# Kernel tuning notes

Hardware: AMD Instinct MI355X
Metric: run time of the kernel (lower is better)

Reference implementation:

```python
import jax, jax.numpy as jnp
import numpy as np

BS = 8
SP_IN, DN_IN = 256, 128
SP_OUT, DN_OUT = 512, 256
N_STK, N_STK_PNT = 32, 64
COOR = 64
SP_NEAR, DN_NEAR = 2, 10
BN_EPS = 1e-5


def _act(x):
    return jax.nn.leaky_relu(x, 0.2)


def _bn(x, g, b, axes):
    # training-mode batch norm over `axes`, per channel (axis 1)
    m = x.mean(axes, keepdims=True)
    v = x.var(axes, keepdims=True)
    shp = [1] * x.ndim
    shp[1] = x.shape[1]
    return g.reshape(shp) * (x - m) * jax.lax.rsqrt(v + BN_EPS) + b.reshape(shp)


def _conv2d(x, w, b, stride, pad_w):
    # x [B,C,H,W], w [O,I,1,kw]
    y = jax.lax.conv_general_dilated(
        x, w, window_strides=stride, padding=[(0, 0), (pad_w, pad_w)],
        dimension_numbers=('NCHW', 'OIHW', 'NCHW'))
    return y + b[None, :, None, None]


def _sq_dist(a, b):
    # a [B,N,C], b [B,M,C] -> [B,N,M]
    return (jnp.sum(a * a, -1)[:, :, None] + jnp.sum(b * b, -1)[:, None, :]
            - 2.0 * jnp.einsum('bnc,bmc->bnm', a, b))


def _index_points(p, idx):
    # p [B,N,C], idx [B,...] -> [B,...,C]
    B = p.shape[0]
    bidx = jnp.arange(B).reshape((B,) + (1,) * (idx.ndim - 1))
    return p[bidx, idx]


def _fps(x, m):
    # deterministic farthest point sampling, start at index 0. x [B,N,D] -> [B,m]
    B, N, _ = x.shape
    bar = jnp.arange(B)

    def step(carry, _):
        dist, far = carry
        cen = x[bar, far]                       # [B,D]
        d = jnp.sum((x - cen[:, None, :]) ** 2, -1)
        dist = jnp.minimum(dist, d)
        return (dist, jnp.argmax(dist, -1).astype(jnp.int32)), far

    init = (jnp.full((B, N), 1e10, x.dtype), jnp.zeros((B,), jnp.int32))
    _, idx = jax.lax.scan(step, init, None, length=m)
    return idx.T  # [B,m]


def _gcn(x, W, b, g, be, k):
    # DGCNN-style EdgeConv: knn in feature space, edge feat [x_j - x_i, x_i],
    # shared 1x1 conv + BN + act, max over neighbors. x [B,C,N] -> [B,O,N]
    xt = jnp.transpose(x, (0, 2, 1))            # [B,N,C]
    d = _sq_dist(xt, xt)
    _, idx = jax.lax.top_k(-d, k)               # [B,N,k] (includes self)
    neigh = _index_points(xt, idx)              # [B,N,k,C]
    cen = xt[:, :, None, :]
    edge = jnp.concatenate([neigh - cen, jnp.broadcast_to(cen, neigh.shape)], -1)
    h = jnp.einsum('bnkc,oc->bonk', edge, W) + b[None, :, None, None]
    h = _act(_bn(h, g, be, (0, 2, 3)))
    return jnp.max(h, axis=3)                   # [B,O,N]


def _forward(sparse_fea, dense_fea, stk_coor,
             d2s_w, d2s_b, d2s_g, d2s_be,
             gsp_w, gsp_b, gsp_g, gsp_be,
             gdn_w, gdn_b, gdn_g, gdn_be,
             dcv_w, dcv_b, dcv_g, dcv_be):
    bs = sparse_fea.shape[0]
    dn4 = dense_fea.reshape(bs, DN_IN, N_STK, N_STK_PNT)

    # DenseToSparse: conv (1,3) valid, BN, act, max over points -> concat
    h = _act(_bn(_conv2d(dn4, d2s_w, d2s_b, (1, 1), 0), d2s_g, d2s_be, (0, 2, 3)))
    sp_from_dn = jnp.max(h, axis=3)                       # [bs,DN_IN,N_STK]
    union_sparse = jnp.concatenate([sparse_fea, sp_from_dn], 1)

    # SparseToDense: broadcast stroke feature onto its points -> concat
    dn_from_sp = jnp.repeat(sparse_fea[:, :, :, None], N_STK_PNT, axis=3)
    union_dense = jnp.concatenate([dn4, dn_from_sp], 1).reshape(
        bs, SP_IN + DN_IN, N_STK * N_STK_PNT)

    # graph updates
    union_sparse = _gcn(union_sparse, gsp_w, gsp_b, gsp_g, gsp_be, SP_NEAR)   # [bs,SP_OUT,N_STK]
    union_dense = _gcn(union_dense, gdn_w, gdn_b, gdn_g, gdn_be, DN_NEAR)     # [bs,DN_OUT,N_pnt]

    # DownSample: FPS over strokes, gather, strided conv halves point count
    fps_idx = _fps(stk_coor, N_STK // 2)                  # [bs,N_STK//2]
    stk_coor_s = _index_points(stk_coor, fps_idx)         # [bs,N_STK//2,COOR]
    sp = jnp.transpose(_index_points(jnp.transpose(union_sparse, (0, 2, 1)), fps_idx), (0, 2, 1))

    emb_d = union_dense.shape[1]
    dn = union_dense.reshape(bs, emb_d, N_STK, N_STK_PNT).transpose(0, 2, 3, 1)
    dn = dn.reshape(bs, N_STK, N_STK_PNT * emb_d)
    dn = _index_points(dn, fps_idx)                       # gather whole strokes
    dn = dn.reshape(bs, N_STK // 2, N_STK_PNT, emb_d).transpose(0, 3, 1, 2)
    dn = _act(_bn(_conv2d(dn, dcv_w, dcv_b, (1, 2), 1), dcv_g, dcv_be, (0, 2, 3)))
    dn = dn.reshape(bs, dn.shape[1], (N_STK // 2) * (N_STK_PNT // 2))
    return sp, dn, stk_coor_s


def setup_inputs() -> dict:
    key = jax.random.key(0)
    ks = jax.random.split(key, 8)
    C_u = SP_IN + DN_IN

    def rn(k, shape, s=0.05):
        return jax.random.normal(k, shape, jnp.float32) * s

    return {
        'sparse_fea': jax.random.normal(ks[0], (BS, SP_IN, N_STK), jnp.float32),
        'dense_fea': jax.random.normal(ks[1], (BS, DN_IN, N_STK * N_STK_PNT), jnp.float32),
        'stk_coor': jax.random.normal(ks[2], (BS, N_STK, COOR), jnp.float32),
        'd2s_w': rn(ks[3], (DN_IN, DN_IN, 1, 3)), 'd2s_b': jnp.zeros(DN_IN),
        'd2s_g': jnp.ones(DN_IN), 'd2s_be': jnp.zeros(DN_IN),
        'gsp_w': rn(ks[4], (SP_OUT, 2 * C_u)), 'gsp_b': jnp.zeros(SP_OUT),
        'gsp_g': jnp.ones(SP_OUT), 'gsp_be': jnp.zeros(SP_OUT),
        'gdn_w': rn(ks[5], (DN_OUT, 2 * C_u)), 'gdn_b': jnp.zeros(DN_OUT),
        'gdn_g': jnp.ones(DN_OUT), 'gdn_be': jnp.zeros(DN_OUT),
        'dcv_w': rn(ks[6], (DN_OUT, DN_OUT, 1, 3)), 'dcv_b': jnp.zeros(DN_OUT),
        'dcv_g': jnp.ones(DN_OUT), 'dcv_be': jnp.zeros(DN_OUT),
    }


def reference(sparse_fea, dense_fea, stk_coor,
              d2s_w, d2s_b, d2s_g, d2s_be,
              gsp_w, gsp_b, gsp_g, gsp_be,
              gdn_w, gdn_b, gdn_g, gdn_be,
              dcv_w, dcv_b, dcv_g, dcv_be):
    return _forward(sparse_fea, dense_fea, stk_coor,
                    d2s_w, d2s_b, d2s_g, d2s_be,
                    gsp_w, gsp_b, gsp_g, gsp_be,
                    gdn_w, gdn_b, gdn_g, gdn_be,
                    dcv_w, dcv_b, dcv_g, dcv_be)
```

## Files before the change

kernel.cpp:

```cpp
#include <hip/hip_runtime.h>

#define NPTS 2048
#define CUF 384

__device__ __forceinline__ float lrelu(float y){ return y>=0.f ? y : 0.2f*y; }

#define GLD16(g, l) __builtin_amdgcn_global_load_lds( \
    (const __attribute__((address_space(1))) void*)(g), \
    (__attribute__((address_space(3))) void*)(l), 16, 0, 0)

__global__ void k_build_xdn(const float* __restrict__ dense,
                            const float* __restrict__ sparse,
                            float* __restrict__ X){
  int b = blockIdx.y, ch = blockIdx.x;
  int t = threadIdx.x;
  __shared__ float tile[64*128];
  for (int k=0;k<32;k++){
    int f = t + k*256;
    int c = f>>6, j = f&63;
    tile[j*128 + c] = dense[((size_t)b*128 + c)*NPTS + ch*64 + j];
  }
  __syncthreads();
  for (int k=0;k<32;k++){
    int f = t + k*256;
    int j = f>>7, c = f&127;
    X[((size_t)b*NPTS + ch*64 + j)*CUF + c] = tile[f];
  }
  float v = sparse[((size_t)b*256 + t)*32 + ch];
  for (int j=0;j<64;j++) X[((size_t)b*NPTS + ch*64 + j)*CUF + 128 + t] = v;
}

__global__ void k_sn(const float* __restrict__ X, float* __restrict__ sn){
  int g = blockIdx.x*256 + threadIdx.x;
  if (g >= 8*NPTS) return;
  const float* row = X + (size_t)g*CUF;
  float blk[4];
  #pragma unroll
  for (int bI=0;bI<4;bI++){
    const float* p = row + bI*96;
    float r[8];
    #pragma unroll
    for (int l=0;l<8;l++) r[l] = __fmul_rn(p[l], p[l]);
    #pragma unroll 1
    for (int i=8;i<96;i+=8){
      #pragma unroll
      for (int l=0;l<8;l++) r[l] = __fadd_rn(r[l], __fmul_rn(p[i+l], p[i+l]));
    }
    float s01 = __fadd_rn(r[0], r[1]);
    float s23 = __fadd_rn(r[2], r[3]);
    float s45 = __fadd_rn(r[4], r[5]);
    float s67 = __fadd_rn(r[6], r[7]);
    blk[bI] = __fadd_rn(__fadd_rn(s01, s23), __fadd_rn(s45, s67));
  }
  sn[g] = __fadd_rn(__fadd_rn(blk[0], blk[1]), __fadd_rn(blk[2], blk[3]));
}

__global__ __launch_bounds__(256) void k_dist_tri(
    const float* __restrict__ X, float* __restrict__ Dot, int b_base){
  int z = blockIdx.z; int b = b_base + z;
  int t = threadIdx.x;
  int tx = t & 15, ty = t >> 4;
  int idx = blockIdx.x, rb = 0;
  while (idx >= 16 - rb){ idx -= 16 - rb; rb++; }
  int cb = rb + idx;
  __shared__ float U[8576];
  float* Xr = U;
  float* Xc = U + 4096;
  float* Ds = U;
  int r0 = rb*128;
  int c0 = cb*128;
  const size_t xb = (size_t)b*NPTS*CUF;
  const size_t zb = (size_t)z*NPTS*NPTS;

  int wv  = t >> 6;
  int sub = (t & 63) >> 3;
  int gs  = t & 7;
  int rowsA[4]; int swzA[4];
  #pragma unroll
  for (int cc=0;cc<4;cc++){
    int grp = wv*4 + cc;
    int row = grp*8 + sub;
    rowsA[cc] = row;
    swzA[cc] = 4*(gs ^ (row&7));
  }

  float acc[8][8];
  #pragma unroll
  for (int i=0;i<8;i++){
    #pragma unroll
    for (int j=0;j<8;j++) acc[i][j] = 0.f;
  }
  for (int kt=0; kt<12; kt++){
    int k0 = kt*32;
    __syncthreads();
    #pragma unroll
    for (int cc=0;cc<4;cc++){
      int grp = wv*4 + cc;
      GLD16(X + xb + (size_t)(r0+rowsA[cc])*CUF + k0 + swzA[cc], Xr + grp*256);
      GLD16(X + xb + (size_t)(c0+rowsA[cc])*CUF + k0 + swzA[cc], Xc + grp*256);
    }
    __syncthreads();
    #pragma unroll
    for (int kk=0; kk<32; kk+=4){
      int G = kk>>2;
      float4 aa[8], bb[8];
      #pragma unroll
      for (int i=0;i<8;i++){ int r = ty+16*i; aa[i] = *(const float4*)&Xr[r*32 + 4*(G ^ (r&7))]; }
      #pragma unroll
      for (int j=0;j<8;j++){ int r = tx+16*j; bb[j] = *(const float4*)&Xc[r*32 + 4*(G ^ (r&7))]; }
      #pragma unroll
      for (int i=0;i<8;i++){
        #pragma unroll
        for (int j=0;j<8;j++){
          float a_ = acc[i][j];
          a_ = fmaf(aa[i].x, bb[j].x, a_);
          a_ = fmaf(aa[i].y, bb[j].y, a_);
          a_ = fmaf(aa[i].z, bb[j].z, a_);
          a_ = fmaf(aa[i].w, bb[j].w, a_);
          acc[i][j] = a_;
        }
      }
    }
  }
  #pragma unroll
  for (int i=0;i<8;i++){
    size_t rbase = zb + (size_t)(r0 + ty + 16*i)*NPTS + c0;
    #pragma unroll
    for (int j=0;j<8;j++) Dot[rbase + tx + 16*j] = acc[i][j];
  }
  if (rb != cb){
    for (int h=0; h<2; h++){
      __syncthreads();
      #pragma unroll
      for (int i2=0;i2<4;i2++){
        #pragma unroll
        for (int j=0;j<8;j++){
          Ds[(tx+16*j)*67 + ty + 16*i2] = acc[h*4+i2][j];
        }
      }
      __syncthreads();
      for (int e=t; e<128*64; e+=256){
        int col = e>>6, rr = e&63;
        Dot[zb + (size_t)(c0+col)*NPTS + r0 + h*64 + rr] = Ds[col*67 + rr];
      }
    }
  }
}

__global__ __launch_bounds__(256) void k_sel(const float* __restrict__ Dot,
                                             const float* __restrict__ sn,
                                             int* __restrict__ idx, int b_base){
  int t = threadIdx.x;
  int lane = t & 63, w = t >> 6;
  int rglob = blockIdx.x*4 + w;
  int bb = rglob >> 11;
  int r  = rglob & 2047;
  int b  = b_base + bb;
  const float* drow = Dot + ((size_t)bb*NPTS + r)*NPTS;
  const float* snp  = sn + (size_t)b*NPTS;
  float snr = snp[r];
  unsigned long long key[32];
  #pragma unroll
  for (int k=0;k<8;k++){
    int cbase = k*256 + lane*4;
    float4 dd = *(const float4*)&drow[cbase];
    float4 ss = *(const float4*)&snp[cbase];
    float v0 = __fsub_rn(__fadd_rn(snr, ss.x), __fmul_rn(2.0f, dd.x));
    float v1 = __fsub_rn(__fadd_rn(snr, ss.y), __fmul_rn(2.0f, dd.y));
    float v2 = __fsub_rn(__fadd_rn(snr, ss.z), __fmul_rn(2.0f, dd.z));
    float v3 = __fsub_rn(__fadd_rn(snr, ss.w), __fmul_rn(2.0f, dd.w));
    float vv[4] = {v0, v1, v2, v3};
    #pragma unroll
    for (int u=0;u<4;u++){
      unsigned int bits = __float_as_uint(vv[u]);
      unsigned int flip = bits ^ ((unsigned int)((int)bits >> 31) | 0x80000000u);
      key[k*4+u] = ((unsigned long long)flip << 32) | (unsigned int)(cbase + u);
    }
  }
  unsigned long long last = 0ull;
  int out[10];
  #pragma unroll
  for (int q=0;q<10;q++){
    const unsigned long long INF = 0xFFFFFFFFFFFFFFFFull;
    unsigned long long m0[16];
    #pragma unroll
    for (int s=0;s<16;s++){
      unsigned long long a = (key[s]    > last) ? key[s]    : INF;
      unsigned long long c = (key[s+16] > last) ? key[s+16] : INF;
      m0[s] = (c < a) ? c : a;
    }
    #pragma unroll
    for (int s=0;s<8;s++) m0[s] = (m0[s+8] < m0[s]) ? m0[s+8] : m0[s];
    #pragma unroll
    for (int s=0;s<4;s++) m0[s] = (m0[s+4] < m0[s]) ? m0[s+4] : m0[s];
    m0[0] = (m0[2] < m0[0]) ? m0[2] : m0[0];
    m0[1] = (m0[3] < m0[1]) ? m0[3] : m0[1];
    unsigned long long m = (m0[1] < m0[0]) ? m0[1] : m0[0];
    #pragma unroll
    for (int sh=1; sh<64; sh<<=1){
      unsigned long long o = (unsigned long long)__shfl_xor((long long)m, sh, 64);
      m = (o < m) ? o : m;
    }
    last = m;
    out[q] = (int)(m & 0xFFFFFFFFull);
  }
  if (lane == 0){
    int* o = idx + ((size_t)b*NPTS + r)*10;
    #pragma unroll
    for (int q=0;q<10;q++) o[q] = out[q];
  }
}

__global__ void k_prepw2(const float* __restrict__ gdn_w, const float* __restrict__ gsp_w,
                         float* __restrict__ Wcd, float* __restrict__ Wcs){
  int g = blockIdx.x*256 + threadIdx.x;
  if (g < 512*CUF){
    int o = g / CUF, c = g % CUF;
    float v;
    if (o < 256) v = gdn_w[(size_t)o*768 + c];
    else { int oo = o - 256; v = gdn_w[(size_t)oo*768 + 384 + c] - gdn_w[(size_t)oo*768 + c]; }
    Wcd[g] = v;
  } else {
    int g2 = g - 512*CUF;
    if (g2 < 1024*CUF){
      int o = g2 / CUF, c = g2 % CUF;
      float v;
      if (o < 512) v = gsp_w[(size_t)o*768 + c];
      else { int oo = o - 512; v = gsp_w[(size_t)oo*768 + 384 + c] - gsp_w[(size_t)oo*768 + c]; }
      Wcs[g2] = v;
    }
  }
}

__global__ __launch_bounds__(256) void k_gemm_pq2(const float* __restrict__ A, const float* __restrict__ W,
                         const float* __restrict__ bias, float* __restrict__ OUT){
  int b = blockIdx.z, mb = blockIdx.y, ob = blockIdx.x;
  int t = threadIdx.x; int tx = t&15, ty = t>>4;
  __shared__ float Xa[4096];
  __shared__ float Xw[4096];
  int m0 = mb*128, o0 = ob*128;
  float acc[8][8];
  #pragma unroll
  for (int i=0;i<8;i++){
    #pragma unroll
    for (int j=0;j<8;j++) acc[i][j] = 0.f;
  }
  int wv  = t >> 6;
  int sub = (t & 63) >> 3;
  int gs  = t & 7;
  int rowsA[4]; int swzA[4];
  #pragma unroll
  for (int cc=0;cc<4;cc++){
    int grp = wv*4 + cc;
    int row = grp*8 + sub;
    rowsA[cc] = row;
    swzA[cc] = 4*(gs ^ (row&7));
  }
  for (int kt=0; kt<12; kt++){
    int k0 = kt*32;
    __syncthreads();
    #pragma unroll
    for (int cc=0;cc<4;cc++){
      int grp = wv*4 + cc;
      GLD16(A + ((size_t)b*NPTS + m0 + rowsA[cc])*CUF + k0 + swzA[cc], Xa + grp*256);
      GLD16(W + (size_t)(o0 + rowsA[cc])*CUF + k0 + swzA[cc], Xw + grp*256);
    }
    __syncthreads();
    #pragma unroll
    for (int kk=0; kk<32; kk+=4){
      int G = kk>>2;
      float4 aa[8], bb[8];
      #pragma unroll
      for (int i=0;i<8;i++){ int r = ty+16*i; aa[i] = *(const float4*)&Xa[r*32 + 4*(G ^ (r&7))]; }
      #pragma unroll
      for (int j=0;j<8;j++){ int r = tx+16*j; bb[j] = *(const float4*)&Xw[r*32 + 4*(G ^ (r&7))]; }
      #pragma unroll
      for (int i=0;i<8;i++){
        #pragma unroll
        for (int j=0;j<8;j++){
          float a_ = acc[i][j];
          a_ = fmaf(aa[i].x, bb[j].x, a_);
          a_ = fmaf(aa[i].y, bb[j].y, a_);
          a_ = fmaf(aa[i].z, bb[j].z, a_);
          a_ = fmaf(aa[i].w, bb[j].w, a_);
          acc[i][j] = a_;
        }
      }
    }
  }
  #pragma unroll
  for (int i=0;i<8;i++){
    int m = m0 + ty + 16*i;
    #pragma unroll
    for (int j=0;j<8;j++){
      int o = o0 + tx + 16*j;
      float v = acc[i][j];
      if (o >= 256) v += bias[o - 256];
      OUT[((size_t)b*NPTS + m)*512 + o] = v;
    }
  }
}

__global__ __launch_bounds__(256) void k_gemm_pq(const float* __restrict__ A, const float* __restrict__ W,
                         const float* __restrict__ bias,
                         float* __restrict__ OUT, int M, int Ototal, int Ohalf){
  int b = blockIdx.z, mb = blockIdx.y, ob = blockIdx.x;
  int t = threadIdx.x; int tr = t&15, tc = t>>4;
  __shared__ float At[64][68], Wt[64][68];
  int m0 = mb*64, o0 = ob*64;
  float acc[4][4];
  #pragma unroll
  for(int i=0;i<4;i++){
    #pragma unroll
    for(int j=0;j<4;j++) acc[i][j]=0.f;
  }
  int li = t>>2, lk = (t&3)*16;
  for (int kt=0;kt<6;kt++){
    int k0 = kt*64;
    {
      int m = m0 + li;
      if (m < M){
        const float4* p = (const float4*)(A + ((size_t)b*M + m)*CUF + k0 + lk);
        #pragma unroll
        for (int e=0;e<4;e++) *(float4*)&At[li][lk+e*4] = p[e];
      } else {
        float4 z = make_float4(0.f,0.f,0.f,0.f);
        #pragma unroll
        for (int e=0;e<4;e++) *(float4*)&At[li][lk+e*4] = z;
      }
      const float4* pw = (const float4*)(W + (size_t)(o0+li)*CUF + k0 + lk);
      #pragma unroll
      for (int e=0;e<4;e++) *(float4*)&Wt[li][lk+e*4] = pw[e];
    }
    __syncthreads();
    #pragma unroll
    for (int k4=0;k4<16;k4++){
      float4 aa[4], bb[4];
      aa[0] = *(const float4*)&At[tr   ][k4*4];
      aa[1] = *(const float4*)&At[tr+16][k4*4];
      aa[2] = *(const float4*)&At[tr+32][k4*4];
      aa[3] = *(const float4*)&At[tr+48][k4*4];
      bb[0] = *(const float4*)&Wt[tc   ][k4*4];
      bb[1] = *(const float4*)&Wt[tc+16][k4*4];
      bb[2] = *(const float4*)&Wt[tc+32][k4*4];
      bb[3] = *(const float4*)&Wt[tc+48][k4*4];
      #pragma unroll
      for(int i=0;i<4;i++){
        #pragma unroll
        for(int j=0;j<4;j++)
          acc[i][j] += aa[i].x*bb[j].x + aa[i].y*bb[j].y + aa[i].z*bb[j].z + aa[i].w*bb[j].w;
      }
    }
    __syncthreads();
  }
  #pragma unroll
  for(int i=0;i<4;i++){
    int m = m0 + tr + 16*i;
    if (m < M){
      #pragma unroll
      for(int j=0;j<4;j++){
        int o = o0 + tc + 16*j;
        float v = acc[i][j];
        if (o >= Ohalf) v += bias[o - Ohalf];
        OUT[((size_t)b*M + m)*Ototal + o] = v;
      }
    }
  }
}

__global__ __launch_bounds__(256) void k_gather_dn(const float* __restrict__ PQ, const int* __restrict__ idx,
                            float* __restrict__ dmax, float* __restrict__ dmin, double* __restrict__ part){
  int b = blockIdx.y, nb = blockIdx.x; int t = threadIdx.x;
  __shared__ int sidx[640];
  int n0 = nb*64;
  for (int k=t; k<640; k+=256) sidx[k] = idx[((size_t)b*NPTS + n0)*10 + k] & 2047;
  __syncthreads();
  double s=0.0, s2=0.0;
  const size_t pb = (size_t)b*NPTS*512;
  for (int n=0;n<64;n++){
    float qv = PQ[pb + (size_t)(n0+n)*512 + 256 + t];
    float mx = -3.4e38f, mn = 3.4e38f;
    #pragma unroll
    for (int k=0;k<10;k++){
      int m = sidx[n*10+k];
      float h = PQ[pb + (size_t)m*512 + t] + qv;
      mx = fmaxf(mx,h); mn = fminf(mn,h);
      s += h; s2 += (double)h*(double)h;
    }
    dmax[((size_t)b*NPTS + n0+n)*256 + t] = mx;
    dmin[((size_t)b*NPTS + n0+n)*256 + t] = mn;
  }
  size_t blk = (size_t)b*32 + nb;
  part[(blk*256 + t)*2] = s; part[(blk*256 + t)*2+1] = s2;
}

__global__ void k_reduce(const double* __restrict__ part, float* __restrict__ mv,
                         int nblk, int C, int count){
  int c = blockIdx.x; int t = threadIdx.x;
  double s=0.0, s2=0.0;
  for (int k=t;k<nblk;k+=64){ s += part[((size_t)k*C+c)*2]; s2 += part[((size_t)k*C+c)*2+1]; }
  #pragma unroll
  for (int off=32; off>=1; off>>=1){ s += __shfl_down(s, off, 64); s2 += __shfl_down(s2, off, 64); }
  if (t==0){
    double mean = s / (double)count;
    double var = s2 / (double)count - mean*mean;
    mv[c*2] = (float)mean;
    mv[c*2+1] = (float)(1.0 / sqrt(var + 1e-5));
  }
}

__global__ void k_epi(const float* __restrict__ xmin, float* __restrict__ xmax,
                      const float* __restrict__ mv, const float* __restrict__ g,
                      const float* __restrict__ be, int C, size_t total){
  size_t i = (size_t)blockIdx.x*256 + threadIdx.x;
  if (i>=total) return;
  int c = (int)(i % (size_t)C);
  float gg = g[c];
  float x = gg >= 0.f ? xmax[i] : xmin[i];
  float y = gg*(x - mv[c*2])*mv[c*2+1] + be[c];
  xmax[i] = lrelu(y);
}

__global__ __launch_bounds__(128) void k_d2s(const float* __restrict__ dense,
                      const float* __restrict__ w, const float* __restrict__ bias,
                      float* __restrict__ mx, float* __restrict__ mn, double* __restrict__ part){
  int b = blockIdx.y, s = blockIdx.x; int t = threadIdx.x;
  __shared__ float IN[128*64];
  for (int k=0;k<64;k++){
    int f = t + k*128;
    int ci = f>>6, wj = f&63;
    IN[f] = dense[((size_t)b*128 + ci)*NPTS + s*64 + wj];
  }
  __syncthreads();
  float acc[62];
  float bv = bias[t];
  #pragma unroll
  for (int wj=0;wj<62;wj++) acc[wj]=bv;
  for (int ci=0;ci<128;ci++){
    const float* wp = w + ((size_t)t*128 + ci)*3;
    float w0 = wp[0], w1 = wp[1], w2 = wp[2];
    const float* row = &IN[ci*64];
    #pragma unroll
    for (int wj=0;wj<62;wj++) acc[wj] += row[wj]*w0 + row[wj+1]*w1 + row[wj+2]*w2;
  }
  float vmx=-3.4e38f, vmn=3.4e38f; double ss=0.0, ss2=0.0;
  #pragma unroll
  for (int wj=0;wj<62;wj++){ float v = acc[wj]; vmx=fmaxf(vmx,v); vmn=fminf(vmn,v); ss+=v; ss2+=(double)v*(double)v; }
  mx[((size_t)b*32+s)*128 + t] = vmx;
  mn[((size_t)b*32+s)*128 + t] = vmn;
  part[(((size_t)b*32+s)*128 + t)*2] = ss; part[(((size_t)b*32+s)*128 + t)*2+1] = ss2;
}

__global__ void k_build_xs(const float* __restrict__ sparse,
                           const float* __restrict__ mx, const float* __restrict__ mn,
                           const float* __restrict__ mv, const float* __restrict__ g,
                           const float* __restrict__ be, float* __restrict__ Xs){
  int b = blockIdx.x; int c = threadIdx.x;
  for (int n=0;n<32;n++){
    float v;
    if (c < 256) v = sparse[((size_t)b*256 + c)*32 + n];
    else {
      int cc = c-256;
      float gg = g[cc];
      float x = gg>=0.f ? mx[((size_t)b*32+n)*128+cc] : mn[((size_t)b*32+n)*128+cc];
      v = lrelu(gg*(x - mv[cc*2])*mv[cc*2+1] + be[cc]);
    }
    Xs[((size_t)b*32+n)*384 + c] = v;
  }
}

__global__ __launch_bounds__(256) void k_knn_sp(const float* __restrict__ Xs, int* __restrict__ idx){
  int b = blockIdx.x; int t = threadIdx.x;
  __shared__ float Xh[32*388];
  __shared__ float snl[32];
  __shared__ float D[32*33];
  for (int k=t;k<32*384;k+=256){ int n=k/384, c=k-n*384; Xh[n*388+c] = Xs[(size_t)b*32*384 + k]; }
  __syncthreads();
  if (t<32){ double s=0.0; for (int c=0;c<384;c++){ double v=(double)Xh[t*388+c]; s+=v*v; } snl[t]=(float)s; }
  __syncthreads();
  for (int p=t;p<1024;p+=256){
    int n=p>>5, m=p&31;
    const float* A=&Xh[n*388]; const float* B=&Xh[m*388];
    double s=0.0;
    for (int c=0;c<384;c++) s += (double)A[c]*(double)B[c];
    D[n*33+m] = (float)((double)snl[m] - 2.0*s);
  }
  __syncthreads();
  if (t<32){
    float v0=3.4e38f,v1=3.4e38f; int i0=0,i1=0;
    for (int m=0;m<32;m++){
      float v=D[t*33+m];
      if (v < v0){ v1=v0;i1=i0; v0=v;i0=m; }
      else if (v < v1){ v1=v;i1=m; }
    }
    idx[((size_t)b*32+t)*2]=i0; idx[((size_t)b*32+t)*2+1]=i1;
  }
}

__global__ void k_gather_sp(const float* __restrict__ PQ, const int* __restrict__ idx,
                            float* __restrict__ umax, float* __restrict__ umin, double* __restrict__ part){
  int b = blockIdx.x; int t = threadIdx.x;
  double s=0.0, s2=0.0;
  for (int n=0;n<32;n++){
    float qv = PQ[((size_t)b*32+n)*1024 + 512 + t];
    float mxv=-3.4e38f, mnv=3.4e38f;
    #pragma unroll
    for (int k=0;k<2;k++){
      int m = idx[((size_t)b*32+n)*2+k] & 31;
      float h = PQ[((size_t)b*32+m)*1024 + t] + qv;
      mxv=fmaxf(mxv,h); mnv=fminf(mnv,h); s+=h; s2+=(double)h*(double)h;
    }
    umax[((size_t)b*32+n)*512+t]=mxv; umin[((size_t)b*32+n)*512+t]=mnv;
  }
  part[((size_t)b*512+t)*2]=s; part[((size_t)b*512+t)*2+1]=s2;
}

__global__ void k_fps(const float* __restrict__ coor, int* __restrict__ fps){
  int b = blockIdx.x; int t = threadIdx.x;
  __shared__ float C[32*64]; __shared__ float dist[32]; __shared__ int fs;
  for (int k=t;k<2048;k+=64) C[k] = coor[(size_t)b*2048 + k];
  if (t<32) dist[t]=1e10f;
  if (t==0) fs=0;
  __syncthreads();
  for (int it=0; it<16; it++){
    int f = fs;
    if (t==0) fps[b*16+it] = f;
    if (t<32){
      float d=0.f;
      for (int c=0;c<64;c++){ float df = C[t*64+c]-C[f*64+c]; d += df*df; }
      dist[t] = fminf(dist[t], d);
    }
    __syncthreads();
    if (t==0){
      float bd=-1.f; int bi=0;
      for (int n=0;n<32;n++){ if (dist[n]>bd){bd=dist[n];bi=n;} }
      fs=bi;
    }
    __syncthreads();
  }
}

__global__ void k_outs(const float* __restrict__ usp, const float* __restrict__ coor,
                       const int* __restrict__ fps, float* __restrict__ out0, float* __restrict__ out2){
  int g = blockIdx.x*256 + threadIdx.x;
  if (g < 65536){
    int b = g >> 13; int rem = g & 8191; int t = rem >> 4; int s = rem & 15;
    int n = fps[b*16+s] & 31;
    out0[((size_t)b*512 + t)*16 + s] = usp[((size_t)b*32+n)*512 + t];
  } else {
    int e = g - 65536;
    if (e < 8192){
      int b = e >> 10; int r = e & 1023; int s = r>>6, c = r&63;
      out2[(size_t)b*1024 + r] = coor[((size_t)b*32 + (fps[b*16+s]&31))*64 + c];
    }
  }
}

__global__ __launch_bounds__(256) void k_dcv(const float* __restrict__ gdn, const int* __restrict__ fps,
                      const float* __restrict__ w, const float* __restrict__ bias,
                      float* __restrict__ pre, double* __restrict__ part){
  int s = blockIdx.x, qg = blockIdx.y, b = blockIdx.z; int t = threadIdx.x;
  __shared__ float I[17*256];
  int n0 = (fps[b*16+s] & 31)*64;
  const size_t gbase = ((size_t)b*NPTS + n0)*256;
  for (int e=t; e<17*256; e+=256){
    int lp = e>>8, c = e&255;
    int p = 16*qg - 1 + lp;
    I[e] = (p >= 0) ? gdn[gbase + (size_t)p*256 + c] : 0.f;
  }
  __syncthreads();
  float acc[8];
  float bv = bias[t];
  #pragma unroll
  for (int q=0;q<8;q++) acc[q]=bv;
  for (int ci=0; ci<256; ci+=4){
    float wv[4][3];
    const float* wp = w + ((size_t)t*256 + ci)*3;
    #pragma unroll
    for (int u=0;u<4;u++){ wv[u][0]=wp[u*3]; wv[u][1]=wp[u*3+1]; wv[u][2]=wp[u*3+2]; }
    #pragma unroll
    for (int q=0;q<8;q++){
      float4 a0 = *(const float4*)&I[(2*q  )*256 + ci];
      float4 a1 = *(const float4*)&I[(2*q+1)*256 + ci];
      float4 a2 = *(const float4*)&I[(2*q+2)*256 + ci];
      acc[q] += a0.x*wv[0][0] + a0.y*wv[1][0] + a0.z*wv[2][0] + a0.w*wv[3][0];
      acc[q] += a1.x*wv[0][1] + a1.y*wv[1][1] + a1.z*wv[2][1] + a1.w*wv[3][1];
      acc[q] += a2.x*wv[0][2] + a2.y*wv[1][2] + a2.z*wv[2][2] + a2.w*wv[3][2];
    }
  }
  double ss=0.0, ss2=0.0;
  #pragma unroll
  for (int q=0;q<8;q++){ ss += acc[q]; ss2 += (double)acc[q]*(double)acc[q]; }
  float* o = pre + (((size_t)b*256 + t)*16 + s)*32 + qg*8;
  #pragma unroll
  for (int q=0;q<8;q++) o[q] = acc[q];
  size_t blk = ((size_t)b*16 + s)*4 + qg;
  part[(blk*256 + t)*2] = ss; part[(blk*256 + t)*2+1] = ss2;
}

__global__ void k_epi_dcv(const float* __restrict__ pre, const float* __restrict__ mv,
                          const float* __restrict__ g, const float* __restrict__ be,
                          float* __restrict__ out1){
  size_t i = (size_t)blockIdx.x*256 + threadIdx.x;
  int c = (int)((i>>9) & 255);
  float gg = g[c];
  float y = gg*(pre[i]-mv[c*2])*mv[c*2+1] + be[c];
  out1[i] = lrelu(y);
}

extern "C" void kernel_launch(void* const* d_in, const int* in_sizes, int n_in,
                              void* d_out, int out_size, void* d_ws, size_t ws_size,
                              hipStream_t stream){
  const float* sparse = (const float*)d_in[0];
  const float* dense  = (const float*)d_in[1];
  const float* coor   = (const float*)d_in[2];
  const float* d2s_w  = (const float*)d_in[3];
  const float* d2s_b  = (const float*)d_in[4];
  const float* d2s_g  = (const float*)d_in[5];
  const float* d2s_be = (const float*)d_in[6];
  const float* gsp_w  = (const float*)d_in[7];
  const float* gsp_b  = (const float*)d_in[8];
  const float* gsp_g  = (const float*)d_in[9];
  const float* gsp_be = (const float*)d_in[10];
  const float* gdn_w  = (const float*)d_in[11];
  const float* gdn_b  = (const float*)d_in[12];
  const float* gdn_g  = (const float*)d_in[13];
  const float* gdn_be = (const float*)d_in[14];
  const float* dcv_w  = (const float*)d_in[15];
  const float* dcv_b  = (const float*)d_in[16];
  const float* dcv_g  = (const float*)d_in[17];
  const float* dcv_be = (const float*)d_in[18];

  float* out0 = (float*)d_out;
  float* out1 = out0 + 8*512*16;
  float* out2 = out1 + (size_t)8*256*512;

  char* base = (char*)d_ws; size_t off = 0;
  auto alloc = [&](size_t bytes)->void*{ void* p = base + off; off += (bytes + 255) & ~(size_t)255; return p; };
  float* Xdn  = (float*)alloc((size_t)8*2048*384*4);
  float* sn   = (float*)alloc((size_t)8*2048*4);
  int*   idxd = (int*)alloc((size_t)8*2048*10*4);
  float* PQ   = (float*)alloc((size_t)8*2048*512*4);
  float* dmax = (float*)alloc((size_t)8*2048*256*4);
  float* dmin = (float*)alloc((size_t)8*2048*256*4);
  double* partdn = (double*)alloc((size_t)256*256*2*8);
  float* mvdn = (float*)alloc(256*2*4);
  float* Wcd  = (float*)alloc((size_t)512*384*4);
  float* Wcs  = (float*)alloc((size_t)1024*384*4);
  float* Xs   = (float*)alloc((size_t)8*32*384*4);
  int*   idxs = (int*)alloc(8*32*2*4);
  float* PQs  = (float*)alloc((size_t)8*32*1024*4);
  float* umax = (float*)alloc((size_t)8*32*512*4);
  float* umin = (float*)alloc((size_t)8*32*512*4);
  double* partsp = (double*)alloc((size_t)8*512*2*8);
  float* mvsp = (float*)alloc(512*2*4);
  float* d2mx = (float*)alloc((size_t)8*32*128*4);
  float* d2mn = (float*)alloc((size_t)8*32*128*4);
  double* partd2 = (double*)alloc((size_t)256*128*2*8);
  float* mvd2 = (float*)alloc(128*2*4);
  int* fps = (int*)alloc(8*16*4);
  float* dcvpre = (float*)alloc((size_t)8*256*512*4);
  double* partdcv = (double*)alloc((size_t)512*256*2*8);
  float* mvdcv = (float*)alloc(256*2*4);
  if (off > ws_size) return;

  size_t dotBytes = (size_t)8*NPTS*NPTS*4;
  float* Dot8 = (off + dotBytes <= ws_size) ? (float*)(base + off) : nullptr;
  float* Dot4 = PQ;

  k_build_xdn<<<dim3(32,8), 256, 0, stream>>>(dense, sparse, Xdn);
  k_sn<<<64, 256, 0, stream>>>(Xdn, sn);
  if (Dot8){
    k_dist_tri<<<dim3(136,1,8), 256, 0, stream>>>(Xdn, Dot8, 0);
    k_sel<<<4096, 256, 0, stream>>>(Dot8, sn, idxd, 0);
  } else {
    k_dist_tri<<<dim3(136,1,4), 256, 0, stream>>>(Xdn, Dot4, 0);
    k_sel<<<2048, 256, 0, stream>>>(Dot4, sn, idxd, 0);
    k_dist_tri<<<dim3(136,1,4), 256, 0, stream>>>(Xdn, Dot4, 4);
    k_sel<<<2048, 256, 0, stream>>>(Dot4, sn, idxd, 4);
  }
  k_prepw2<<<2304, 256, 0, stream>>>(gdn_w, gsp_w, Wcd, Wcs);
  k_gemm_pq2<<<dim3(4,16,8), 256, 0, stream>>>(Xdn, Wcd, gdn_b, PQ);
  k_gather_dn<<<dim3(32,8), 256, 0, stream>>>(PQ, idxd, dmax, dmin, partdn);
  k_reduce<<<256, 64, 0, stream>>>(partdn, mvdn, 256, 256, 163840);
  k_epi<<<16384, 256, 0, stream>>>(dmin, dmax, mvdn, gdn_g, gdn_be, 256, (size_t)8*2048*256);
  k_d2s<<<dim3(32,8), 128, 0, stream>>>(dense, d2s_w, d2s_b, d2mx, d2mn, partd2);
  k_reduce<<<128, 64, 0, stream>>>(partd2, mvd2, 256, 128, 15872);
  k_build_xs<<<8, 384, 0, stream>>>(sparse, d2mx, d2mn, mvd2, d2s_g, d2s_be, Xs);
  k_knn_sp<<<8, 256, 0, stream>>>(Xs, idxs);
  k_gemm_pq<<<dim3(16,1,8), 256, 0, stream>>>(Xs, Wcs, gsp_b, PQs, 32, 1024, 512);
  k_gather_sp<<<8, 512, 0, stream>>>(PQs, idxs, umax, umin, partsp);
  k_reduce<<<512, 64, 0, stream>>>(partsp, mvsp, 8, 512, 512);
  k_epi<<<512, 256, 0, stream>>>(umin, umax, mvsp, gsp_g, gsp_be, 512, (size_t)8*32*512);
  k_fps<<<8, 64, 0, stream>>>(coor, fps);
  k_outs<<<288, 256, 0, stream>>>(umax, coor, fps, out0, out2);
  k_dcv<<<dim3(16,4,8), 256, 0, stream>>>(dmax, fps, dcv_w, dcv_b, dcvpre, partdcv);
  k_reduce<<<256, 64, 0, stream>>>(partdcv, mvdcv, 512, 256, 4096);
  k_epi_dcv<<<4096, 256, 0, stream>>>(dcvpre, mvdcv, dcv_g, dcv_be, out1);
}
```

Baseline: 695.3 us.

## Double-buffer LDS tiles in distance GEMM and fuse norm epilogue into it

The triangular distance kernel now double-buffers its LDS tiles, issuing the next k-slice's async global-to-LDS loads before computing on the current one, so only one barrier per iteration remains. It also computes the full squared distance (row norm + column norm − 2·dot) in the epilogue from norms cached in shared memory. This removes the per-element norm loads and arithmetic from the selection kernel. LDS use roughly doubles, which may lower occupancy. The double buffer also relies on async loads completing before the single barrier.

```diff
diff --git a/kernel.cpp b/kernel.cpp
--- a/kernel.cpp
+++ b/kernel.cpp
@@ -56,21 +56,22 @@
 }
 
 __global__ __launch_bounds__(256) void k_dist_tri(
-    const float* __restrict__ X, float* __restrict__ Dot, int b_base){
+    const float* __restrict__ X, const float* __restrict__ sn,
+    float* __restrict__ Dmat, int b_base){
   int z = blockIdx.z; int b = b_base + z;
   int t = threadIdx.x;
   int tx = t & 15, ty = t >> 4;
   int idx = blockIdx.x, rb = 0;
   while (idx >= 16 - rb){ idx -= 16 - rb; rb++; }
   int cb = rb + idx;
-  __shared__ float U[8576];
-  float* Xr = U;
-  float* Xc = U + 4096;
-  float* Ds = U;
+  __shared__ float BUF[16384];
+  __shared__ float snr_s[128], snc_s[128];
   int r0 = rb*128;
   int c0 = cb*128;
   const size_t xb = (size_t)b*NPTS*CUF;
   const size_t zb = (size_t)z*NPTS*NPTS;
+  const size_t snb = (size_t)b*NPTS;
+  if (t < 128){ snr_s[t] = sn[snb + r0 + t]; snc_s[t] = sn[snb + c0 + t]; }
 
   int wv  = t >> 6;
   int sub = (t & 63) >> 3;
@@ -84,22 +85,32 @@
     swzA[cc] = 4*(gs ^ (row&7));
   }
 
-  float acc[8][8];
-  #pragma unroll
-  for (int i=0;i<8;i++){
-    #pragma unroll
-    for (int j=0;j<8;j++) acc[i][j] = 0.f;
-  }
-  for (int kt=0; kt<12; kt++){
+  auto STAGE = [&](int p, int kt){
     int k0 = kt*32;
-    __syncthreads();
+    float* Xr = BUF + p*8192;
+    float* Xc = Xr + 4096;
     #pragma unroll
     for (int cc=0;cc<4;cc++){
       int grp = wv*4 + cc;
       GLD16(X + xb + (size_t)(r0+rowsA[cc])*CUF + k0 + swzA[cc], Xr + grp*256);
       GLD16(X + xb + (size_t)(c0+rowsA[cc])*CUF + k0 + swzA[cc], Xc + grp*256);
     }
-    __syncthreads();
+  };
+
+  float acc[8][8];
+  #pragma unroll
+  for (int i=0;i<8;i++){
+    #pragma unroll
+    for (int j=0;j<8;j++) acc[i][j] = 0.f;
+  }
+  STAGE(0, 0);
+  __syncthreads();
+  #pragma unroll 1
+  for (int s=0; s<12; s++){
+    int p = s & 1;
+    if (s < 11) STAGE(p^1, s+1);
+    const float* Xr = BUF + p*8192;
+    const float* Xc = Xr + 4096;
     #pragma unroll
     for (int kk=0; kk<32; kk+=4){
       int G = kk>>2;
@@ -121,14 +132,24 @@
         }
       }
     }
+    __syncthreads();
+  }
+  #pragma unroll
+  for (int i=0;i<8;i++){
+    float snr_v = snr_s[ty + 16*i];
+    #pragma unroll
+    for (int j=0;j<8;j++){
+      acc[i][j] = __fsub_rn(__fadd_rn(snr_v, snc_s[tx + 16*j]), __fmul_rn(2.0f, acc[i][j]));
+    }
   }
   #pragma unroll
   for (int i=0;i<8;i++){
     size_t rbase = zb + (size_t)(r0 + ty + 16*i)*NPTS + c0;
     #pragma unroll
-    for (int j=0;j<8;j++) Dot[rbase + tx + 16*j] = acc[i][j];
+    for (int j=0;j<8;j++) Dmat[rbase + tx + 16*j] = acc[i][j];
   }
   if (rb != cb){
+    float* Ds = BUF;
     for (int h=0; h<2; h++){
       __syncthreads();
       #pragma unroll
@@ -141,14 +162,13 @@
       __syncthreads();
       for (int e=t; e<128*64; e+=256){
         int col = e>>6, rr = e&63;
-        Dot[zb + (size_t)(c0+col)*NPTS + r0 + h*64 + rr] = Ds[col*67 + rr];
+        Dmat[zb + (size_t)(c0+col)*NPTS + r0 + h*64 + rr] = Ds[col*67 + rr];
       }
     }
   }
 }
 
-__global__ __launch_bounds__(256) void k_sel(const float* __restrict__ Dot,
-                                             const float* __restrict__ sn,
+__global__ __launch_bounds__(256) void k_sel(const float* __restrict__ Dmat,
                                              int* __restrict__ idx, int b_base){
   int t = threadIdx.x;
   int lane = t & 63, w = t >> 6;
@@ -156,20 +176,13 @@
   int bb = rglob >> 11;
   int r  = rglob & 2047;
   int b  = b_base + bb;
-  const float* drow = Dot + ((size_t)bb*NPTS + r)*NPTS;
-  const float* snp  = sn + (size_t)b*NPTS;
-  float snr = snp[r];
+  const float* drow = Dmat + ((size_t)bb*NPTS + r)*NPTS;
   unsigned long long key[32];
   #pragma unroll
   for (int k=0;k<8;k++){
     int cbase = k*256 + lane*4;
     float4 dd = *(const float4*)&drow[cbase];
-    float4 ss = *(const float4*)&snp[cbase];
-    float v0 = __fsub_rn(__fadd_rn(snr, ss.x), __fmul_rn(2.0f, dd.x));
-    float v1 = __fsub_rn(__fadd_rn(snr, ss.y), __fmul_rn(2.0f, dd.y));
-    float v2 = __fsub_rn(__fadd_rn(snr, ss.z), __fmul_rn(2.0f, dd.z));
-    float v3 = __fsub_rn(__fadd_rn(snr, ss.w), __fmul_rn(2.0f, dd.w));
-    float vv[4] = {v0, v1, v2, v3};
+    float vv[4] = {dd.x, dd.y, dd.z, dd.w};
     #pragma unroll
     for (int u=0;u<4;u++){
       unsigned int bits = __float_as_uint(vv[u]);
@@ -671,13 +684,13 @@
   k_build_xdn<<<dim3(32,8), 256, 0, stream>>>(dense, sparse, Xdn);
   k_sn<<<64, 256, 0, stream>>>(Xdn, sn);
   if (Dot8){
-    k_dist_tri<<<dim3(136,1,8), 256, 0, stream>>>(Xdn, Dot8, 0);
-    k_sel<<<4096, 256, 0, stream>>>(Dot8, sn, idxd, 0);
+    k_dist_tri<<<dim3(136,1,8), 256, 0, stream>>>(Xdn, sn, Dot8, 0);
+    k_sel<<<4096, 256, 0, stream>>>(Dot8, idxd, 0);
   } else {
-    k_dist_tri<<<dim3(136,1,4), 256, 0, stream>>>(Xdn, Dot4, 0);
-    k_sel<<<2048, 256, 0, stream>>>(Dot4, sn, idxd, 0);
-    k_dist_tri<<<dim3(136,1,4), 256, 0, stream>>>(Xdn, Dot4, 4);
-    k_sel<<<2048, 256, 0, stream>>>(Dot4, sn, idxd, 4);
+    k_dist_tri<<<dim3(136,1,4), 256, 0, stream>>>(Xdn, sn, Dot4, 0);
+    k_sel<<<2048, 256, 0, stream>>>(Dot4, idxd, 0);
+    k_dist_tri<<<dim3(136,1,4), 256, 0, stream>>>(Xdn, sn, Dot4, 4);
+    k_sel<<<2048, 256, 0, stream>>>(Dot4, idxd, 4);
   }
   k_prepw2<<<2304, 256, 0, stream>>>(gdn_w, gsp_w, Wcd, Wcs);
   k_gemm_pq2<<<dim3(4,16,8), 256, 0, stream>>>(Xdn, Wcd, gdn_b, PQ);
```

New measurement: 791.7 us. 1.14x slower.
